# Kernel optimization log

Measured on AMD Instinct MI355X. Metric: run time of the kernel, lower is better.

Reference implementation:

```python
import jax, jax.numpy as jnp
import numpy as np

# dims: B=4 batch, S=512 seq, P=128 input_size, C=64 classes(=hidden_size), K=64 gln layer width, 4 context bits -> 16 contexts
B, S, P, C, K, NBITS = 4, 512, 128, 64, 64, 4
NCTX = 2 ** NBITS
LOGIT_CLIP = 5.0


def setup_inputs() -> dict:
    key = jax.random.key(0)
    ks = jax.random.split(key, 8)
    return {
        "x": jax.random.normal(ks[0], (B, S, P), jnp.float32),
        "hidden": jax.random.normal(ks[1], (B, C), jnp.float32),
        # GLN layer 1: per-class, per-neuron halfspace context hyperplanes and gated weights
        "H1": jax.random.normal(ks[2], (C, K, NBITS, P), jnp.float32),
        "W1": jax.random.normal(ks[3], (C, K, NCTX, P), jnp.float32) / np.sqrt(P),
        # GLN output layer: one neuron per class
        "H2": jax.random.normal(ks[4], (C, NBITS, P), jnp.float32),
        "W2": jax.random.normal(ks[5], (C, NCTX, K), jnp.float32) / np.sqrt(K),
        # fc2: Linear(input_size, hidden_size)
        "fc2_w": jax.random.normal(ks[6], (C, P), jnp.float32) / np.sqrt(P),
        "fc2_b": jnp.zeros((C,), jnp.float32),
    }


def _ctx_index(bits):
    # bits: (..., NBITS) bool -> integer context id in [0, 2^NBITS)
    return (bits * (2 ** jnp.arange(NBITS, dtype=jnp.int32))).sum(-1)


def _gln_predict(x, H1, W1, H2, W2):
    # base predictions: sigmoid(x) -> logit space is x itself (clipped for stability)
    l0 = jnp.clip(x, -LOGIT_CLIP, LOGIT_CLIP)  # (B,S,P)
    # layer 1: halfspace gating then geometric mixing in logit space
    ctx1 = _ctx_index(jnp.einsum('bsp,ckjp->bsckj', x, H1) > 0)          # (B,S,C,K)
    mix1 = jnp.einsum('bsp,ckxp->bsckx', l0, W1)                          # (B,S,C,K,NCTX)
    l1 = jnp.take_along_axis(mix1, ctx1[..., None], axis=-1)[..., 0]      # (B,S,C,K)
    l1 = jnp.clip(l1, -LOGIT_CLIP, LOGIT_CLIP)
    # output layer: one gated neuron per class
    ctx2 = _ctx_index(jnp.einsum('bsp,cjp->bscj', x, H2) > 0)             # (B,S,C)
    mix2 = jnp.einsum('bsck,cxk->bscx', l1, W2)                           # (B,S,C,NCTX)
    l2 = jnp.take_along_axis(mix2, ctx2[..., None], axis=-1)[..., 0]      # (B,S,C)
    return jax.nn.sigmoid(l2)


def reference(x, hidden, H1, W1, H2, W2, fc2_w, fc2_b):
    b = _gln_predict(x, H1, W1, H2, W2)                   # (B,S,C)
    # multihead gating
    sig_alphas = jax.nn.sigmoid(x @ fc2_w.T + fc2_b)      # (B,S,C)
    b = b * sig_alphas

    # sequential roll+add+relu recurrence over seq_len
    def step(h, bt):
        h = jax.nn.relu(bt + jnp.roll(h, 1, axis=-1))
        return h, h

    h_last, outs = jax.lax.scan(step, hidden, jnp.swapaxes(b, 0, 1))  # outs: (S,B,C)
    outputs = jnp.swapaxes(outs, 0, 1)                                # (B,S,C)
    return outputs, h_last
```

## Files before the change

### kernel.cpp

```cpp
#include <hip/hip_runtime.h>
#include <math.h>

#define BB 4
#define SS 512
#define PP 128
#define CC 64
#define KK 64
#define NCTX_ 16
#define TT 64
#define NTILES ((BB*SS)/TT)

typedef __attribute__((ext_vector_type(8))) short bf16x8;
typedef __attribute__((ext_vector_type(4))) float f32x4;
typedef __attribute__((ext_vector_type(16))) float f32x16;

static __device__ __forceinline__ float bf2f(short h) {
    unsigned u = ((unsigned)(unsigned short)h) << 16;
    return __builtin_bit_cast(float, u);
}
static __device__ __forceinline__ short f2bf(float f) {
    unsigned u = __builtin_bit_cast(unsigned, f);
    unsigned r = (u + 0x7fffu + ((u >> 16) & 1u)) >> 16;
    return (short)(unsigned short)r;
}
static __device__ __forceinline__ bf16x8 clampfrag(bf16x8 h) {
    typedef __attribute__((ext_vector_type(4))) unsigned u32x4;
    u32x4 u = __builtin_bit_cast(u32x4, h);
    #pragma unroll
    for (int i = 0; i < 4; ++i) {
        const unsigned w = u[i];
        const unsigned s = w & 0x80008000u;
        unsigned lo = w & 0x7fffu;
        unsigned hi = (w >> 16) & 0x7fffu;
        lo = lo > 0x40a0u ? 0x40a0u : lo;
        hi = hi > 0x40a0u ? 0x40a0u : hi;
        u[i] = s | lo | (hi << 16);
    }
    return __builtin_bit_cast(bf16x8, u);
}
template <int BASE>
static __device__ __forceinline__ float sel8(const f32x16& a, int sel) {
    return sel == 0 ? a[BASE + 0] : sel == 1 ? a[BASE + 1] :
           sel == 2 ? a[BASE + 2] : sel == 3 ? a[BASE + 3] :
           sel == 4 ? a[BASE + 4] : sel == 5 ? a[BASE + 5] :
           sel == 6 ? a[BASE + 6] : a[BASE + 7];
}

__global__ __launch_bounds__(256) void pack_kernel(
    const float* __restrict__ W1, const float* __restrict__ H1,
    const float* __restrict__ H2, const float* __restrict__ fc2w,
    short* __restrict__ W1h, short* __restrict__ H1h32, short* __restrict__ H1l32,
    short* __restrict__ H2Wh, short* __restrict__ H2Wl)
{
    const int bid  = blockIdx.x;
    const int w    = threadIdx.x >> 6;
    const int lane = threadIdx.x & 63;

    if (bid < 4096) {
        const int gw  = bid * 4 + w;
        const int q8  = gw & 7;
        const int m   = (gw >> 3) & 31;
        const int cc  = gw >> 8;
        const int r   = lane & 31;
        const int k   = 2 * m + (r >> 4);
        const int ctx = r & 15;
        const int col = q8 * 16 + (lane >> 5) * 8;
        const float4* s = reinterpret_cast<const float4*>(
            W1 + (((size_t)(cc * KK + k) * NCTX_ + ctx) * PP + col));
        const float4 a = s[0], b = s[1];
        const float vv[8] = {a.x, a.y, a.z, a.w, b.x, b.y, b.z, b.w};
        bf16x8 hh;
        #pragma unroll
        for (int e = 0; e < 8; ++e) hh[e] = f2bf(vv[e]);
        *reinterpret_cast<bf16x8*>(W1h + ((size_t)gw * 64 + lane) * 8) = hh;
    } else if (bid < 4096 + 1024) {
        const int gw  = (bid - 4096) * 4 + w;
        const int row = (gw >> 3) * 32 + (lane & 31);
        const int col = (gw & 7) * 16 + (lane >> 5) * 8;
        const float4* s = reinterpret_cast<const float4*>(H1 + (size_t)row * PP + col);
        const float4 a = s[0], b = s[1];
        const float vv[8] = {a.x, a.y, a.z, a.w, b.x, b.y, b.z, b.w};
        bf16x8 hh, ll;
        #pragma unroll
        for (int e = 0; e < 8; ++e) {
            const short hv = f2bf(vv[e]);
            hh[e] = hv;
            ll[e] = f2bf(vv[e] - bf2f(hv));
        }
        const size_t o = ((size_t)gw * 64 + lane) * 8;
        *reinterpret_cast<bf16x8*>(H1h32 + o) = hh;
        *reinterpret_cast<bf16x8*>(H1l32 + o) = ll;
    } else {
        const int cidx = bid - (4096 + 1024);
        #pragma unroll
        for (int i = 0; i < 2; ++i) {
            const int q8  = w * 2 + i;
            const int row = lane & 31;
            const int col = q8 * 16 + (lane >> 5) * 8;
            float vv[8];
            if (row < 4) {
                const float4* s = reinterpret_cast<const float4*>(
                    H2 + ((size_t)cidx * 4 + row) * PP + col);
                const float4 a = s[0], b = s[1];
                vv[0]=a.x; vv[1]=a.y; vv[2]=a.z; vv[3]=a.w;
                vv[4]=b.x; vv[5]=b.y; vv[6]=b.z; vv[7]=b.w;
            } else if (row == 4) {
                const float4* s = reinterpret_cast<const float4*>(
                    fc2w + (size_t)cidx * PP + col);
                const float4 a = s[0], b = s[1];
                vv[0]=a.x; vv[1]=a.y; vv[2]=a.z; vv[3]=a.w;
                vv[4]=b.x; vv[5]=b.y; vv[6]=b.z; vv[7]=b.w;
            } else {
                #pragma unroll
                for (int e = 0; e < 8; ++e) vv[e] = 0.f;
            }
            bf16x8 hh, ll;
            #pragma unroll
            for (int e = 0; e < 8; ++e) {
                const short hv = f2bf(vv[e]);
                hh[e] = hv;
                ll[e] = f2bf(vv[e] - bf2f(hv));
            }
            const size_t o = (((size_t)cidx * 8 + q8) * 64 + lane) * 8;
            *reinterpret_cast<bf16x8*>(H2Wh + o) = hh;
            *reinterpret_cast<bf16x8*>(H2Wl + o) = ll;
        }
    }
}

__global__ __launch_bounds__(256, 4) void predict_kernel(
    const float* __restrict__ x,
    const short* __restrict__ H1h32,
    const short* __restrict__ H1l32,
    const short* __restrict__ W1h,
    const short* __restrict__ H2Wh,
    const short* __restrict__ H2Wl,
    const float* __restrict__ W2,
    const float* __restrict__ fc2b,
    float* __restrict__ bout)
{
    __shared__ short xuh[2][8][64][8];
    __shared__ short xul[2][8][64][8];
    __shared__ unsigned char ctxb[TT][68];
    __shared__ unsigned char bit2b[TT];
    __shared__ float af[TT];

    const int tid  = threadIdx.x;
    const int lane = tid & 63;
    const int wid  = __builtin_amdgcn_readfirstlane(tid >> 6);
    const int bid  = blockIdx.x;
    const int sw   = ((bid & 7) << 8) | (bid >> 3);
    const int c    = sw >> 5;
    const int tile = sw & (NTILES - 1);
    const int tok0 = tile * TT;

    const int l31 = lane & 31;
    const int l5  = lane >> 5;
    const f32x16 zero16 = {0.f,0.f,0.f,0.f,0.f,0.f,0.f,0.f,
                           0.f,0.f,0.f,0.f,0.f,0.f,0.f,0.f};

    {
        const int tok = tid >> 2;
        const int qq  = tid & 3;
        const int ct  = tok >> 5;
        const float4* x4 = reinterpret_cast<const float4*>(
            x + (size_t)(tok0 + tok) * PP + qq * 32);
        float v[32];
        #pragma unroll
        for (int i = 0; i < 8; ++i) {
            const float4 t = x4[i];
            v[i*4+0]=t.x; v[i*4+1]=t.y; v[i*4+2]=t.z; v[i*4+3]=t.w;
        }
        #pragma unroll
        for (int gg = 0; gg < 4; ++gg) {
            const int q8 = qq * 2 + (gg >> 1);
            const int lw = (gg & 1) * 32 + (tok & 31);
            bf16x8 hh, ll;
            #pragma unroll
            for (int e = 0; e < 8; ++e) {
                const float f = v[gg*8+e];
                const short hv = f2bf(f);
                hh[e] = hv;
                ll[e] = f2bf(f - bf2f(hv));
            }
            *reinterpret_cast<bf16x8*>(&xuh[ct][q8][lw][0]) = hh;
            *reinterpret_cast<bf16x8*>(&xul[ct][q8][lw][0]) = ll;
        }
    }
    __syncthreads();

    #pragma unroll
    for (int rt = 0; rt < 2; ++rt) {
        f32x16 aA = zero16, aB = zero16;
        const size_t tb = ((size_t)(c * 8 + wid * 2 + rt)) * 8;
        #pragma unroll
        for (int q8 = 0; q8 < 8; ++q8) {
            const size_t fo = ((tb + q8) * 64 + lane) * 8;
            const bf16x8 ah  = *reinterpret_cast<const bf16x8*>(H1h32 + fo);
            const bf16x8 al  = *reinterpret_cast<const bf16x8*>(H1l32 + fo);
            const bf16x8 bh0 = *reinterpret_cast<const bf16x8*>(&xuh[0][q8][lane][0]);
            const bf16x8 bl0 = *reinterpret_cast<const bf16x8*>(&xul[0][q8][lane][0]);
            const bf16x8 bh1 = *reinterpret_cast<const bf16x8*>(&xuh[1][q8][lane][0]);
            const bf16x8 bl1 = *reinterpret_cast<const bf16x8*>(&xul[1][q8][lane][0]);
            aA = __builtin_amdgcn_mfma_f32_32x32x16_bf16(ah, bh0, aA, 0, 0, 0);
            aA = __builtin_amdgcn_mfma_f32_32x32x16_bf16(ah, bl0, aA, 0, 0, 0);
            aA = __builtin_amdgcn_mfma_f32_32x32x16_bf16(al, bh0, aA, 0, 0, 0);
            aB = __builtin_amdgcn_mfma_f32_32x32x16_bf16(ah, bh1, aB, 0, 0, 0);
            aB = __builtin_amdgcn_mfma_f32_32x32x16_bf16(ah, bl1, aB, 0, 0, 0);
            aB = __builtin_amdgcn_mfma_f32_32x32x16_bf16(al, bh1, aB, 0, 0, 0);
        }
        #pragma unroll
        for (int rg = 0; rg < 4; ++rg) {
            const int k = wid * 16 + rt * 8 + 2 * rg + l5;
            const int cvA = (aA[4*rg+0] > 0.f ? 1 : 0) | (aA[4*rg+1] > 0.f ? 2 : 0) |
                            (aA[4*rg+2] > 0.f ? 4 : 0) | (aA[4*rg+3] > 0.f ? 8 : 0);
            const int cvB = (aB[4*rg+0] > 0.f ? 1 : 0) | (aB[4*rg+1] > 0.f ? 2 : 0) |
                            (aB[4*rg+2] > 0.f ? 4 : 0) | (aB[4*rg+3] > 0.f ? 8 : 0);
            ctxb[l31][k]      = (unsigned char)cvA;
            ctxb[32 + l31][k] = (unsigned char)cvB;
        }
    }

    if (wid < 2) {
        f32x16 a2 = zero16;
        #pragma unroll
        for (int q8 = 0; q8 < 8; ++q8) {
            const size_t fo = (((size_t)c * 8 + q8) * 64 + lane) * 8;
            const bf16x8 ah = *reinterpret_cast<const bf16x8*>(H2Wh + fo);
            const bf16x8 al = *reinterpret_cast<const bf16x8*>(H2Wl + fo);
            const bf16x8 bh = *reinterpret_cast<const bf16x8*>(&xuh[wid][q8][lane][0]);
            const bf16x8 bl = *reinterpret_cast<const bf16x8*>(&xul[wid][q8][lane][0]);
            a2 = __builtin_amdgcn_mfma_f32_32x32x16_bf16(ah, bh, a2, 0, 0, 0);
            a2 = __builtin_amdgcn_mfma_f32_32x32x16_bf16(ah, bl, a2, 0, 0, 0);
            a2 = __builtin_amdgcn_mfma_f32_32x32x16_bf16(al, bh, a2, 0, 0, 0);
        }
        const int tok = wid * 32 + l31;
        if (l5 == 0) {
            bit2b[tok] = (unsigned char)((a2[0] > 0.f ? 1 : 0) | (a2[1] > 0.f ? 2 : 0) |
                                         (a2[2] > 0.f ? 4 : 0) | (a2[3] > 0.f ? 8 : 0));
        } else {
            af[tok] = a2[0];
        }
    }
    __syncthreads();

    {
        bf16x8* xp = reinterpret_cast<bf16x8*>(&xuh[0][0][0][0]);
        #pragma unroll
        for (int i = 0; i < 8; ++i) {
            const int idx = i * 256 + tid;
            xp[idx] = clampfrag(xp[idx]);
        }
    }
    __syncthreads();

    short* l1s = &xul[0][0][0][0];
    {
        #pragma unroll 2
        for (int m = 0; m < 8; ++m) {
            const int pr = wid * 8 + m;
            const int k0 = 2 * pr, k1 = 2 * pr + 1;
            f32x16 a0 = zero16, a1 = zero16;
            #pragma unroll
            for (int q8 = 0; q8 < 8; ++q8) {
                const size_t fo = (((size_t)(c * 32 + pr) * 8 + q8) * 64 + lane) * 8;
                const bf16x8 ah = *reinterpret_cast<const bf16x8*>(W1h + fo);
                const bf16x8 b0 = *reinterpret_cast<const bf16x8*>(&xuh[0][q8][lane][0]);
                const bf16x8 b1 = *reinterpret_cast<const bf16x8*>(&xuh[1][q8][lane][0]);
                a0 = __builtin_amdgcn_mfma_f32_32x32x16_bf16(ah, b0, a0, 0, 0, 0);
                a1 = __builtin_amdgcn_mfma_f32_32x32x16_bf16(ah, b1, a1, 0, 0, 0);
            }
            #pragma unroll
            for (int ct = 0; ct < 2; ++ct) {
                const f32x16& av = ct ? a1 : a0;
                const int tok = ct * 32 + l31;
                const int cx0 = ctxb[tok][k0];
                const int cx1 = ctxb[tok][k1];
                if (l5 == ((cx0 >> 2) & 1)) {
                    const float v = sel8<0>(av, (cx0 & 3) + ((cx0 >> 3) << 2));
                    l1s[tok * 68 + k0] = f2bf(fminf(fmaxf(v, -5.f), 5.f));
                }
                if (l5 == ((cx1 >> 2) & 1)) {
                    const float v = sel8<8>(av, (cx1 & 3) + ((cx1 >> 3) << 2));
                    l1s[tok * 68 + k1] = f2bf(fminf(fmaxf(v, -5.f), 5.f));
                }
            }
        }
    }
    __syncthreads();

    {
        const int tok = tid >> 2;
        const int qt  = tid & 3;
        const int ctx2 = bit2b[tok];
        const float4* w2p = reinterpret_cast<const float4*>(
            W2 + ((size_t)c * NCTX_ + ctx2) * KK + qt * 16);
        float s = 0.f;
        #pragma unroll
        for (int i4 = 0; i4 < 4; ++i4) {
            const float4 w = w2p[i4];
            const int kb = tok * 68 + qt * 16 + i4 * 4;
            s = fmaf(w.x, bf2f(l1s[kb + 0]),
                fmaf(w.y, bf2f(l1s[kb + 1]),
                fmaf(w.z, bf2f(l1s[kb + 2]),
                fmaf(w.w, bf2f(l1s[kb + 3]), s))));
        }
        s += __shfl_xor(s, 1, 64);
        s += __shfl_xor(s, 2, 64);
        if (qt == 0) {
            const float alpha = af[tok] + fc2b[c];
            const float bv = (1.f / (1.f + expf(-s))) * (1.f / (1.f + expf(-alpha)));
            bout[(size_t)(tok0 + tok) * CC + c] = bv;
        }
    }
}

__global__ __launch_bounds__(256, 4) void predict_fb_kernel(
    const float* __restrict__ x,
    const float* __restrict__ H1,
    const float* __restrict__ W1b,
    const float* __restrict__ H2,
    const float* __restrict__ W2,
    const float* __restrict__ fc2w,
    const float* __restrict__ fc2b,
    float* __restrict__ bout)
{
    __shared__ float xs[PP][TT + 1];
    __shared__ float bitss[4][TT];
    __shared__ float apart[4][TT];
    __shared__ float l2part[4][TT];

    const int tid  = threadIdx.x;
    const int lane = tid & 63;
    const int wid  = __builtin_amdgcn_readfirstlane(tid >> 6);
    const int bid  = blockIdx.x;
    const int sw   = ((bid & 7) << 8) | (bid >> 3);
    const int c    = sw >> 5;
    const int tile = sw & (NTILES - 1);
    const int tok0 = tile * TT;

    {
        const float4* xg = reinterpret_cast<const float4*>(x + (size_t)tok0 * PP);
        #pragma unroll
        for (int it = 0; it < (TT * PP / 4) / 256; ++it) {
            const int i = it * 256 + tid;
            const float4 v = xg[i];
            const int t = i >> 5;
            const int p = (i & 31) << 2;
            xs[p + 0][t] = v.x; xs[p + 1][t] = v.y;
            xs[p + 2][t] = v.z; xs[p + 3][t] = v.w;
        }
    }
    __syncthreads();

    int ctxreg[16];
    {
        const float4* H1c4 = reinterpret_cast<const float4*>(H1 + (size_t)c * KK * 4 * PP);
        #pragma unroll
        for (int gg = 0; gg < 8; ++gg) {
            const int k = wid * 16 + gg * 2;
            const float4* h4 = H1c4 + (size_t)k * 4 * 32;
            float acc[8] = {0.f, 0.f, 0.f, 0.f, 0.f, 0.f, 0.f, 0.f};
            #pragma unroll 2
            for (int p4 = 0; p4 < 32; ++p4) {
                const float x0 = xs[4 * p4 + 0][lane];
                const float x1 = xs[4 * p4 + 1][lane];
                const float x2 = xs[4 * p4 + 2][lane];
                const float x3 = xs[4 * p4 + 3][lane];
                #pragma unroll
                for (int r = 0; r < 8; ++r) {
                    const float4 w = h4[r * 32 + p4];
                    acc[r] = fmaf(w.w, x3, fmaf(w.z, x2, fmaf(w.y, x1, fmaf(w.x, x0, acc[r]))));
                }
            }
            ctxreg[gg * 2]     = (acc[0] > 0.f ? 1 : 0) | (acc[1] > 0.f ? 2 : 0) |
                                 (acc[2] > 0.f ? 4 : 0) | (acc[3] > 0.f ? 8 : 0);
            ctxreg[gg * 2 + 1] = (acc[4] > 0.f ? 1 : 0) | (acc[5] > 0.f ? 2 : 0) |
                                 (acc[6] > 0.f ? 4 : 0) | (acc[7] > 0.f ? 8 : 0);
        }
    }
    {
        const float4* h2 = reinterpret_cast<const float4*>(H2 + ((size_t)c * 4 + wid) * PP);
        float d = 0.f;
        #pragma unroll 8
        for (int p4 = 0; p4 < 32; ++p4) {
            const float4 w = h2[p4];
            d = fmaf(w.w, xs[4 * p4 + 3][lane], fmaf(w.z, xs[4 * p4 + 2][lane],
                fmaf(w.y, xs[4 * p4 + 1][lane], fmaf(w.x, xs[4 * p4 + 0][lane], d))));
        }
        bitss[wid][lane] = (d > 0.f) ? 1.f : 0.f;
        const float4* fw = reinterpret_cast<const float4*>(fc2w + (size_t)c * PP) + wid * 8;
        float ap = 0.f;
        #pragma unroll
        for (int p4 = 0; p4 < 8; ++p4) {
            const float4 w = fw[p4];
            const int p = wid * 32 + 4 * p4;
            ap = fmaf(w.w, xs[p + 3][lane], fmaf(w.z, xs[p + 2][lane],
                 fmaf(w.y, xs[p + 1][lane], fmaf(w.x, xs[p + 0][lane], ap))));
        }
        apart[wid][lane] = ap;
    }
    __syncthreads();

    float l1v[16];
    {
        const float4* W1c4 = reinterpret_cast<const float4*>(W1b) +
                             (size_t)(c * KK + wid * 16) * 512;
        #pragma unroll
        for (int gg = 0; gg < 2; ++gg) {
            float s[8] = {0.f, 0.f, 0.f, 0.f, 0.f, 0.f, 0.f, 0.f};
            const float4* wp[8];
            #pragma unroll
            for (int jj = 0; jj < 8; ++jj) {
                const int kk = gg * 8 + jj;
                wp[jj] = W1c4 + (size_t)kk * 512 + (size_t)ctxreg[kk] * 32;
            }
            #pragma unroll 2
            for (int p4 = 0; p4 < 32; ++p4) {
                const float x0 = fminf(fmaxf(xs[4 * p4 + 0][lane], -5.f), 5.f);
                const float x1 = fminf(fmaxf(xs[4 * p4 + 1][lane], -5.f), 5.f);
                const float x2 = fminf(fmaxf(xs[4 * p4 + 2][lane], -5.f), 5.f);
                const float x3 = fminf(fmaxf(xs[4 * p4 + 3][lane], -5.f), 5.f);
                #pragma unroll
                for (int jj = 0; jj < 8; ++jj) {
                    const float4 wv = wp[jj][p4];
                    s[jj] = fmaf(wv.w, x3, fmaf(wv.z, x2, fmaf(wv.y, x1, fmaf(wv.x, x0, s[jj]))));
                }
            }
            #pragma unroll
            for (int jj = 0; jj < 8; ++jj)
                l1v[gg * 8 + jj] = fminf(fmaxf(s[jj], -5.f), 5.f);
        }
    }
    {
        const int ctx2 = (bitss[0][lane] > 0.5f ? 1 : 0) | (bitss[1][lane] > 0.5f ? 2 : 0) |
                         (bitss[2][lane] > 0.5f ? 4 : 0) | (bitss[3][lane] > 0.5f ? 8 : 0);
        const float* w2 = W2 + ((size_t)c * NCTX_ + ctx2) * KK + wid * 16;
        float lp = 0.f;
        #pragma unroll
        for (int jj = 0; jj < 16; ++jj) lp = fmaf(w2[jj], l1v[jj], lp);
        l2part[wid][lane] = lp;
    }
    __syncthreads();
    if (wid == 0) {
        const int t = lane;
        const float l2 = (l2part[0][t] + l2part[1][t]) + (l2part[2][t] + l2part[3][t]);
        const float alpha = apart[0][t] + apart[1][t] + apart[2][t] + apart[3][t] + fc2b[c];
        const float bv = (1.f / (1.f + expf(-l2))) * (1.f / (1.f + expf(-alpha)));
        bout[(size_t)(tok0 + t) * CC + c] = bv;
    }
}

__global__ __launch_bounds__(64) void scan_kernel(const float* __restrict__ hidden,
                                                  float* __restrict__ out)
{
    const int b    = blockIdx.x;
    const int lane = threadIdx.x;
    float* row = out + (size_t)b * SS * CC;
    const float hprev = hidden[b * CC + ((lane + 63) & 63)];

    float nb[64];
    #pragma unroll
    for (int j = 0; j < 64; ++j) nb[j] = row[j * CC + ((lane + j) & 63)];
    float acc = fmaxf(nb[0] + hprev, 0.f);
    row[lane] = acc;
    #pragma unroll
    for (int j = 1; j < 64; ++j) {
        acc += nb[j];
        row[j * CC + ((lane + j) & 63)] = acc;
    }
    for (int c0 = 64; c0 < SS; c0 += 64) {
        #pragma unroll
        for (int j = 0; j < 64; ++j)
            nb[j] = row[(c0 + j) * CC + ((lane + c0 + j) & 63)];
        #pragma unroll
        for (int j = 0; j < 64; ++j) {
            acc += nb[j];
            row[(c0 + j) * CC + ((lane + c0 + j) & 63)] = acc;
        }
    }
    out[(size_t)BB * SS * CC + b * CC + ((lane + 63) & 63)] = acc;
}

extern "C" void kernel_launch(void* const* d_in, const int* in_sizes, int n_in,
                              void* d_out, int out_size, void* d_ws, size_t ws_size,
                              hipStream_t stream) {
    const float* x      = (const float*)d_in[0];
    const float* hidden = (const float*)d_in[1];
    const float* H1     = (const float*)d_in[2];
    const float* W1     = (const float*)d_in[3];
    const float* H2     = (const float*)d_in[4];
    const float* W2     = (const float*)d_in[5];
    const float* fc2w   = (const float*)d_in[6];
    const float* fc2b   = (const float*)d_in[7];
    float* out = (float*)d_out;

    const size_t MB = 1024 * 1024;

    if (ws_size >= 25 * MB) {
        short* W1hp  = (short*)d_ws;
        short* H1hp  = (short*)((char*)d_ws + 16 * MB);
        short* H1lp  = (short*)((char*)d_ws + 20 * MB);
        short* H2Whp = (short*)((char*)d_ws + 24 * MB);
        short* H2Wlp = (short*)((char*)d_ws + 24 * MB + 512 * 1024);
        pack_kernel<<<dim3(4096 + 1024 + CC), 256, 0, stream>>>(
            W1, H1, H2, fc2w, W1hp, H1hp, H1lp, H2Whp, H2Wlp);
        predict_kernel<<<dim3(CC * NTILES), 256, 0, stream>>>(
            x, H1hp, H1lp, W1hp, H2Whp, H2Wlp, W2, fc2b, out);
    } else {
        predict_fb_kernel<<<dim3(CC * NTILES), 256, 0, stream>>>(
            x, H1, W1, H2, W2, fc2w, fc2b, out);
    }
    scan_kernel<<<dim3(BB), 64, 0, stream>>>(hidden, out);
}
```

Baseline: 107.7 us.

## Pre-split x into bf16 hi/lo fragments in pack kernel and read from global

```diff
diff --git a/kernel.cpp b/kernel.cpp
--- a/kernel.cpp
+++ b/kernel.cpp
@@ -49,8 +49,10 @@
 __global__ __launch_bounds__(256) void pack_kernel(
     const float* __restrict__ W1, const float* __restrict__ H1,
     const float* __restrict__ H2, const float* __restrict__ fc2w,
+    const float* __restrict__ x,
     short* __restrict__ W1h, short* __restrict__ H1h32, short* __restrict__ H1l32,
-    short* __restrict__ H2Wh, short* __restrict__ H2Wl)
+    short* __restrict__ H2Wh, short* __restrict__ H2Wl,
+    short* __restrict__ xph, short* __restrict__ xpl)
 {
     const int bid  = blockIdx.x;
     const int w    = threadIdx.x >> 6;
@@ -90,7 +92,7 @@
         const size_t o = ((size_t)gw * 64 + lane) * 8;
         *reinterpret_cast<bf16x8*>(H1h32 + o) = hh;
         *reinterpret_cast<bf16x8*>(H1l32 + o) = ll;
-    } else {
+    } else if (bid < 4096 + 1024 + CC) {
         const int cidx = bid - (4096 + 1024);
         #pragma unroll
         for (int i = 0; i < 2; ++i) {
@@ -125,11 +127,32 @@
             *reinterpret_cast<bf16x8*>(H2Wh + o) = hh;
             *reinterpret_cast<bf16x8*>(H2Wl + o) = ll;
         }
-    }
-}
-
-__global__ __launch_bounds__(256, 4) void predict_kernel(
-    const float* __restrict__ x,
+    } else {
+        const int frag = (bid - (4096 + 1024 + CC)) * 4 + w;
+        const int tile = frag >> 4;
+        const int ct   = (frag >> 3) & 1;
+        const int q8   = frag & 7;
+        const int row  = tile * 64 + ct * 32 + (lane & 31);
+        const int col  = q8 * 16 + (lane >> 5) * 8;
+        const float4* s = reinterpret_cast<const float4*>(x + (size_t)row * PP + col);
+        const float4 a = s[0], b = s[1];
+        const float vv[8] = {a.x, a.y, a.z, a.w, b.x, b.y, b.z, b.w};
+        bf16x8 hh, ll;
+        #pragma unroll
+        for (int e = 0; e < 8; ++e) {
+            const short hv = f2bf(vv[e]);
+            hh[e] = hv;
+            ll[e] = f2bf(vv[e] - bf2f(hv));
+        }
+        const size_t o = ((size_t)frag * 64 + lane) * 8;
+        *reinterpret_cast<bf16x8*>(xph + o) = hh;
+        *reinterpret_cast<bf16x8*>(xpl + o) = ll;
+    }
+}
+
+__global__ __launch_bounds__(256, 5) void predict_kernel(
+    const short* __restrict__ xph,
+    const short* __restrict__ xpl,
     const short* __restrict__ H1h32,
     const short* __restrict__ H1l32,
     const short* __restrict__ W1h,
@@ -139,8 +162,8 @@
     const float* __restrict__ fc2b,
     float* __restrict__ bout)
 {
-    __shared__ short xuh[2][8][64][8];
-    __shared__ short xul[2][8][64][8];
+    __shared__ short xc[2][8][64][8];
+    __shared__ short l1s[TT][68];
     __shared__ unsigned char ctxb[TT][68];
     __shared__ unsigned char bit2b[TT];
     __shared__ float af[TT];
@@ -160,35 +183,17 @@
                            0.f,0.f,0.f,0.f,0.f,0.f,0.f,0.f};
 
     {
-        const int tok = tid >> 2;
-        const int qq  = tid & 3;
-        const int ct  = tok >> 5;
-        const float4* x4 = reinterpret_cast<const float4*>(
-            x + (size_t)(tok0 + tok) * PP + qq * 32);
-        float v[32];
-        #pragma unroll
-        for (int i = 0; i < 8; ++i) {
-            const float4 t = x4[i];
-            v[i*4+0]=t.x; v[i*4+1]=t.y; v[i*4+2]=t.z; v[i*4+3]=t.w;
-        }
-        #pragma unroll
-        for (int gg = 0; gg < 4; ++gg) {
-            const int q8 = qq * 2 + (gg >> 1);
-            const int lw = (gg & 1) * 32 + (tok & 31);
-            bf16x8 hh, ll;
-            #pragma unroll
-            for (int e = 0; e < 8; ++e) {
-                const float f = v[gg*8+e];
-                const short hv = f2bf(f);
-                hh[e] = hv;
-                ll[e] = f2bf(f - bf2f(hv));
-            }
-            *reinterpret_cast<bf16x8*>(&xuh[ct][q8][lw][0]) = hh;
-            *reinterpret_cast<bf16x8*>(&xul[ct][q8][lw][0]) = ll;
+        const bf16x8* src = reinterpret_cast<const bf16x8*>(xph) + tile * 1024;
+        bf16x8* dst = reinterpret_cast<bf16x8*>(&xc[0][0][0][0]);
+        #pragma unroll
+        for (int i = 0; i < 4; ++i) {
+            const int idx = i * 256 + tid;
+            dst[idx] = clampfrag(src[idx]);
         }
     }
     __syncthreads();
 
+    const size_t xb = (size_t)tile * 16 * 64 * 8;
     #pragma unroll
     for (int rt = 0; rt < 2; ++rt) {
         f32x16 aA = zero16, aB = zero16;
@@ -198,10 +203,12 @@
             const size_t fo = ((tb + q8) * 64 + lane) * 8;
             const bf16x8 ah  = *reinterpret_cast<const bf16x8*>(H1h32 + fo);
             const bf16x8 al  = *reinterpret_cast<const bf16x8*>(H1l32 + fo);
-            const bf16x8 bh0 = *reinterpret_cast<const bf16x8*>(&xuh[0][q8][lane][0]);
-            const bf16x8 bl0 = *reinterpret_cast<const bf16x8*>(&xul[0][q8][lane][0]);
-            const bf16x8 bh1 = *reinterpret_cast<const bf16x8*>(&xuh[1][q8][lane][0]);
-            const bf16x8 bl1 = *reinterpret_cast<const bf16x8*>(&xul[1][q8][lane][0]);
+            const size_t b0o = xb + ((size_t)q8 * 64 + lane) * 8;
+            const size_t b1o = xb + ((size_t)(8 + q8) * 64 + lane) * 8;
+            const bf16x8 bh0 = *reinterpret_cast<const bf16x8*>(xph + b0o);
+            const bf16x8 bl0 = *reinterpret_cast<const bf16x8*>(xpl + b0o);
+            const bf16x8 bh1 = *reinterpret_cast<const bf16x8*>(xph + b1o);
+            const bf16x8 bl1 = *reinterpret_cast<const bf16x8*>(xpl + b1o);
             aA = __builtin_amdgcn_mfma_f32_32x32x16_bf16(ah, bh0, aA, 0, 0, 0);
             aA = __builtin_amdgcn_mfma_f32_32x32x16_bf16(ah, bl0, aA, 0, 0, 0);
             aA = __builtin_amdgcn_mfma_f32_32x32x16_bf16(al, bh0, aA, 0, 0, 0);
@@ -228,8 +235,9 @@
             const size_t fo = (((size_t)c * 8 + q8) * 64 + lane) * 8;
             const bf16x8 ah = *reinterpret_cast<const bf16x8*>(H2Wh + fo);
             const bf16x8 al = *reinterpret_cast<const bf16x8*>(H2Wl + fo);
-            const bf16x8 bh = *reinterpret_cast<const bf16x8*>(&xuh[wid][q8][lane][0]);
-            const bf16x8 bl = *reinterpret_cast<const bf16x8*>(&xul[wid][q8][lane][0]);
+            const size_t bo = xb + ((size_t)(wid * 8 + q8) * 64 + lane) * 8;
+            const bf16x8 bh = *reinterpret_cast<const bf16x8*>(xph + bo);
+            const bf16x8 bl = *reinterpret_cast<const bf16x8*>(xpl + bo);
             a2 = __builtin_amdgcn_mfma_f32_32x32x16_bf16(ah, bh, a2, 0, 0, 0);
             a2 = __builtin_amdgcn_mfma_f32_32x32x16_bf16(ah, bl, a2, 0, 0, 0);
             a2 = __builtin_amdgcn_mfma_f32_32x32x16_bf16(al, bh, a2, 0, 0, 0);
@@ -242,19 +250,7 @@
             af[tok] = a2[0];
         }
     }
-    __syncthreads();
-
-    {
-        bf16x8* xp = reinterpret_cast<bf16x8*>(&xuh[0][0][0][0]);
-        #pragma unroll
-        for (int i = 0; i < 8; ++i) {
-            const int idx = i * 256 + tid;
-            xp[idx] = clampfrag(xp[idx]);
-        }
-    }
-    __syncthreads();
-
-    short* l1s = &xul[0][0][0][0];
+
     {
         #pragma unroll 2
         for (int m = 0; m < 8; ++m) {
@@ -265,8 +261,8 @@
             for (int q8 = 0; q8 < 8; ++q8) {
                 const size_t fo = (((size_t)(c * 32 + pr) * 8 + q8) * 64 + lane) * 8;
                 const bf16x8 ah = *reinterpret_cast<const bf16x8*>(W1h + fo);
-                const bf16x8 b0 = *reinterpret_cast<const bf16x8*>(&xuh[0][q8][lane][0]);
-                const bf16x8 b1 = *reinterpret_cast<const bf16x8*>(&xuh[1][q8][lane][0]);
+                const bf16x8 b0 = *reinterpret_cast<const bf16x8*>(&xc[0][q8][lane][0]);
+                const bf16x8 b1 = *reinterpret_cast<const bf16x8*>(&xc[1][q8][lane][0]);
                 a0 = __builtin_amdgcn_mfma_f32_32x32x16_bf16(ah, b0, a0, 0, 0, 0);
                 a1 = __builtin_amdgcn_mfma_f32_32x32x16_bf16(ah, b1, a1, 0, 0, 0);
             }
@@ -278,11 +274,11 @@
                 const int cx1 = ctxb[tok][k1];
                 if (l5 == ((cx0 >> 2) & 1)) {
                     const float v = sel8<0>(av, (cx0 & 3) + ((cx0 >> 3) << 2));
-                    l1s[tok * 68 + k0] = f2bf(fminf(fmaxf(v, -5.f), 5.f));
+                    l1s[tok][k0] = f2bf(fminf(fmaxf(v, -5.f), 5.f));
                 }
                 if (l5 == ((cx1 >> 2) & 1)) {
                     const float v = sel8<8>(av, (cx1 & 3) + ((cx1 >> 3) << 2));
-                    l1s[tok * 68 + k1] = f2bf(fminf(fmaxf(v, -5.f), 5.f));
+                    l1s[tok][k1] = f2bf(fminf(fmaxf(v, -5.f), 5.f));
                 }
             }
         }
@@ -299,11 +295,11 @@
         #pragma unroll
         for (int i4 = 0; i4 < 4; ++i4) {
             const float4 w = w2p[i4];
-            const int kb = tok * 68 + qt * 16 + i4 * 4;
-            s = fmaf(w.x, bf2f(l1s[kb + 0]),
-                fmaf(w.y, bf2f(l1s[kb + 1]),
-                fmaf(w.z, bf2f(l1s[kb + 2]),
-                fmaf(w.w, bf2f(l1s[kb + 3]), s))));
+            const int kb = qt * 16 + i4 * 4;
+            s = fmaf(w.x, bf2f(l1s[tok][kb + 0]),
+                fmaf(w.y, bf2f(l1s[tok][kb + 1]),
+                fmaf(w.z, bf2f(l1s[tok][kb + 2]),
+                fmaf(w.w, bf2f(l1s[tok][kb + 3]), s))));
         }
         s += __shfl_xor(s, 1, 64);
         s += __shfl_xor(s, 2, 64);
@@ -497,16 +493,18 @@
 
     const size_t MB = 1024 * 1024;
 
-    if (ws_size >= 25 * MB) {
+    if (ws_size >= 27 * MB) {
         short* W1hp  = (short*)d_ws;
         short* H1hp  = (short*)((char*)d_ws + 16 * MB);
         short* H1lp  = (short*)((char*)d_ws + 20 * MB);
         short* H2Whp = (short*)((char*)d_ws + 24 * MB);
         short* H2Wlp = (short*)((char*)d_ws + 24 * MB + 512 * 1024);
-        pack_kernel<<<dim3(4096 + 1024 + CC), 256, 0, stream>>>(
-            W1, H1, H2, fc2w, W1hp, H1hp, H1lp, H2Whp, H2Wlp);
+        short* xphp  = (short*)((char*)d_ws + 25 * MB);
+        short* xplp  = (short*)((char*)d_ws + 25 * MB + 512 * 1024);
+        pack_kernel<<<dim3(4096 + 1024 + CC + 128), 256, 0, stream>>>(
+            W1, H1, H2, fc2w, x, W1hp, H1hp, H1lp, H2Whp, H2Wlp, xphp, xplp);
         predict_kernel<<<dim3(CC * NTILES), 256, 0, stream>>>(
-            x, H1hp, H1lp, W1hp, H2Whp, H2Wlp, W2, fc2b, out);
+            xphp, xplp, H1hp, H1lp, W1hp, H2Whp, H2Wlp, W2, fc2b, out);
     } else {
         predict_fb_kernel<<<dim3(CC * NTILES), 256, 0, stream>>>(
             x, H1, W1, H2, W2, fc2w, fc2b, out);
```

Result: slower. 136.7 us (+26.9%).
